# Optimization experiments

Measured on AMD Instinct MI355X. Metric: run time of the kernel, lower is better.

The kernel has to match this reference:

```python
import jax, jax.numpy as jnp
import numpy as np

N_LEVELS = 8
FEAT = 4
BASE = 512.0
MAX_RES = 32768.0
PLS_LOG2 = np.log2(MAX_RES / BASE) / (N_LEVELS - 1)  # per_level_scale exponent
PRIMES = (1, 2654435761, 805459861)  # tcnn hash primes
NUM_BASIS = 4
TIME_RES = 8


def grid_encode(x, table):
    """tcnn HashGrid encoding. x: [N, d] in [0,1]; table: [L, T, F]. Returns [N, L*F]."""
    L, T, F = table.shape
    N, d = x.shape
    feats = []
    for l in range(L):
        scale = np.exp2(l * PLS_LOG2) * BASE - 1.0  # tcnn grid_scale
        pos = x * jnp.float32(scale) + 0.5
        p0 = jnp.floor(pos)
        frac = pos - p0  # [N, d]
        p0u = p0.astype(jnp.uint32)
        acc = jnp.zeros((N, F), dtype=table.dtype)
        for corner in range(2 ** d):
            h = jnp.zeros((N,), dtype=jnp.uint32)
            w = jnp.ones((N,), dtype=pos.dtype)
            for j in range(d):
                b = (corner >> j) & 1
                c = p0u[:, j] + jnp.uint32(b)
                h = h ^ (c * jnp.uint32(PRIMES[j]))  # uint32 wraparound, as in tcnn
                w = w * (frac[:, j] if b else (1.0 - frac[:, j]))
            idx = (h & jnp.uint32(T - 1)).astype(jnp.int32)  # T is a power of 2
            acc = acc + w[:, None] * table[l][idx]
        feats.append(acc)
    return jnp.concatenate(feats, axis=-1)  # level-major layout like tcnn


def interp_basis(feat, t):
    """Lagrange multi-basis interpolation over feature chunks. feat: [N, L*F] -> [N, L*F//NUM_BASIS]."""
    N = feat.shape[0]
    f = feat.reshape(N, N_LEVELS, FEAT)
    chunks = jnp.split(f, NUM_BASIS, axis=-1)
    Tn = [i / (NUM_BASIS - 1) for i in range(NUM_BASIS)]
    out = jnp.zeros_like(chunks[0])
    for i in range(NUM_BASIS):
        coef = 1.0
        for m in range(NUM_BASIS):
            if m != i:
                coef = coef * (t - Tn[m]) / (Tn[i] - Tn[m])
        out = out + coef * chunks[i]
    return out.reshape(N, -1)


def hash_grid_t(xp, t, tables):
    """HashGridT: blend two per-time-slice 2D hash encodings, then basis-interp. tables: [TR, L, T, F]."""
    idx = t * (TIME_RES - 1)
    i1 = jnp.floor(idx).astype(jnp.int32)
    i2 = jnp.ceil(idx).astype(jnp.int32)
    w2 = idx - i1.astype(idx.dtype)
    f1 = grid_encode(xp, tables[i1])
    f2 = grid_encode(xp, tables[i2])
    feat = (1.0 - w2) * f1 + w2 * f2  # equals f1 exactly when idx is integral
    return interp_basis(feat, t)


def setup_inputs() -> dict:
    key = jax.random.key(0)
    k1, k2, k3, k4, k5, k6 = jax.random.split(key, 6)
    N = 1_000_000
    x = jax.random.uniform(k1, (N, 3), dtype=jnp.float32)
    t = jax.random.uniform(k2, (), dtype=jnp.float32)
    table_static = jax.random.normal(k3, (N_LEVELS, 2 ** 19, FEAT), dtype=jnp.float32) * 0.1
    table_xy = jax.random.normal(k4, (TIME_RES, N_LEVELS, 2 ** 15, FEAT), dtype=jnp.float32) * 0.1
    table_xz = jax.random.normal(k5, (TIME_RES, N_LEVELS, 2 ** 13, FEAT), dtype=jnp.float32) * 0.1
    table_yz = jax.random.normal(k6, (TIME_RES, N_LEVELS, 2 ** 13, FEAT), dtype=jnp.float32) * 0.1
    return {"x": x, "t": t, "table_static": table_static,
            "table_xy": table_xy, "table_xz": table_xz, "table_yz": table_yz}


def reference(x, t, table_static, table_xy, table_xz, table_yz):
    # static 3D hash grid features: [N, 32]
    feat_static = grid_encode(x, table_static)
    # dynamic tri-plane time features, concat reduction: [N, 24]
    d_xy = hash_grid_t(x[:, (0, 1)], t, table_xy)
    d_xz = hash_grid_t(x[:, (0, 2)], t, table_xz)
    d_yz = hash_grid_t(x[:, (1, 2)], t, table_yz)
    feat_dynamic = jnp.concatenate([d_xy, d_xz, d_yz], axis=-1)
    return feat_static, feat_dynamic  # decompose=True returns the pair
```

## Files before the change

### kernel.cpp

```cpp
#include <hip/hip_runtime.h>
#include <math.h>

#define NLEV 8

struct Scales { float s[NLEV]; };

__device__ __forceinline__ float4 enc2d(float pa, float pb, float s,
                                        const float* __restrict__ tbl,
                                        unsigned mask)
{
    float posa = pa * s + 0.5f;
    float posb = pb * s + 0.5f;
    float fla = floorf(posa), flb = floorf(posb);
    float fra = posa - fla, frb = posb - flb;
    unsigned ua = (unsigned)fla, ub = (unsigned)flb;
    float wa0 = 1.0f - fra, wb0 = 1.0f - frb;
    float4 acc = make_float4(0.f, 0.f, 0.f, 0.f);
#pragma unroll
    for (int c = 0; c < 4; ++c) {
        unsigned ca = ua + (c & 1);
        unsigned cb = ub + ((c >> 1) & 1);
        unsigned h = ca ^ (cb * 2654435761u);
        unsigned idx = h & mask;
        float4 v = *reinterpret_cast<const float4*>(tbl + (size_t)idx * 4u);
        float w = ((c & 1) ? fra : wa0) * (((c >> 1) & 1) ? frb : wb0);
        acc.x += w * v.x; acc.y += w * v.y; acc.z += w * v.z; acc.w += w * v.w;
    }
    return acc;
}

__global__ __launch_bounds__(256) void hg4d_kernel(
    const float* __restrict__ x,
    const float* __restrict__ tptr,
    const float* __restrict__ tstat,
    const float* __restrict__ txy,
    const float* __restrict__ txz,
    const float* __restrict__ tyz,
    float* __restrict__ outs,
    float* __restrict__ outd,
    int N, Scales sc)
{
    int n = blockIdx.x * blockDim.x + threadIdx.x;
    if (n >= N) return;
    float x0 = x[3 * (size_t)n + 0];
    float x1 = x[3 * (size_t)n + 1];
    float x2 = x[3 * (size_t)n + 2];
    float t = tptr[0];

#pragma unroll
    for (int l = 0; l < NLEV; ++l) {
        float s = sc.s[l];
        float p0 = x0 * s + 0.5f, p1 = x1 * s + 0.5f, p2 = x2 * s + 0.5f;
        float q0 = floorf(p0), q1 = floorf(p1), q2 = floorf(p2);
        float f0 = p0 - q0, f1 = p1 - q1, f2 = p2 - q2;
        unsigned u0 = (unsigned)q0, u1 = (unsigned)q1, u2 = (unsigned)q2;
        float g0 = 1.f - f0, g1 = 1.f - f1, g2 = 1.f - f2;
        const float* tb = tstat + (size_t)l * (1u << 19) * 4u;
        float4 acc = make_float4(0.f, 0.f, 0.f, 0.f);
#pragma unroll
        for (int c = 0; c < 8; ++c) {
            unsigned c0 = u0 + (c & 1);
            unsigned c1 = u1 + ((c >> 1) & 1);
            unsigned c2 = u2 + ((c >> 2) & 1);
            unsigned h = c0 ^ (c1 * 2654435761u) ^ (c2 * 805459861u);
            unsigned idx = h & ((1u << 19) - 1u);
            float4 v = *reinterpret_cast<const float4*>(tb + (size_t)idx * 4u);
            float w = ((c & 1) ? f0 : g0) * (((c >> 1) & 1) ? f1 : g1)
                    * (((c >> 2) & 1) ? f2 : g2);
            acc.x += w * v.x; acc.y += w * v.y; acc.z += w * v.z; acc.w += w * v.w;
        }
        *reinterpret_cast<float4*>(outs + (size_t)n * 32u + l * 4u) = acc;
    }

    float idxf = t * 7.0f;
    float fl = floorf(idxf);
    int i1 = (int)fl;
    int i2 = (int)ceilf(idxf);
    float w2 = idxf - fl;
    float w1 = 1.0f - w2;

    float Tn[4] = {0.f, 1.f / 3.f, 2.f / 3.f, 1.f};
    float coef[4];
#pragma unroll
    for (int i = 0; i < 4; ++i) {
        float c = 1.0f;
#pragma unroll
        for (int m = 0; m < 4; ++m)
            if (m != i) c = c * (t - Tn[m]) / (Tn[i] - Tn[m]);
        coef[i] = c;
    }

    float od[24];

    auto plane = [&](float pa, float pb, const float* __restrict__ tbl,
                     unsigned Tsz, int ob) {
        const float* b1 = tbl + (size_t)i1 * NLEV * Tsz * 4u;
        const float* b2 = tbl + (size_t)i2 * NLEV * Tsz * 4u;
#pragma unroll
        for (int l = 0; l < NLEV; ++l) {
            float s = sc.s[l];
            const float* t1 = b1 + (size_t)l * Tsz * 4u;
            const float* t2 = b2 + (size_t)l * Tsz * 4u;
            float4 a = enc2d(pa, pb, s, t1, Tsz - 1u);
            float4 b = enc2d(pa, pb, s, t2, Tsz - 1u);
            float bx = w1 * a.x + w2 * b.x;
            float by = w1 * a.y + w2 * b.y;
            float bz = w1 * a.z + w2 * b.z;
            float bw = w1 * a.w + w2 * b.w;
            float o = coef[0] * bx;
            o = o + coef[1] * by;
            o = o + coef[2] * bz;
            o = o + coef[3] * bw;
            od[ob + l] = o;
        }
    };
    plane(x0, x1, txy, 1u << 15, 0);
    plane(x0, x2, txz, 1u << 13, 8);
    plane(x1, x2, tyz, 1u << 13, 16);

    float* op = outd + (size_t)n * 24u;
#pragma unroll
    for (int k = 0; k < 6; ++k) {
        float4 v = make_float4(od[4 * k], od[4 * k + 1], od[4 * k + 2], od[4 * k + 3]);
        *reinterpret_cast<float4*>(op + 4 * k) = v;
    }
}

extern "C" void kernel_launch(void* const* d_in, const int* in_sizes, int n_in,
                              void* d_out, int out_size, void* d_ws, size_t ws_size,
                              hipStream_t stream) {
    const float* x     = (const float*)d_in[0];
    const float* tptr  = (const float*)d_in[1];
    const float* tstat = (const float*)d_in[2];
    const float* txy   = (const float*)d_in[3];
    const float* txz   = (const float*)d_in[4];
    const float* tyz   = (const float*)d_in[5];
    int N = in_sizes[0] / 3;
    float* outs = (float*)d_out;
    float* outd = outs + (size_t)N * 32u;

    Scales sc;
    const double pls = 6.0 / 7.0;
    for (int l = 0; l < NLEV; ++l)
        sc.s[l] = (float)(exp2((double)l * pls) * 512.0 - 1.0);

    dim3 block(256);
    dim3 grid((N + 255) / 256);
    hipLaunchKernelGGL(hg4d_kernel, grid, block, 0, stream,
                       x, tptr, tstat, txy, txz, tyz, outs, outd, N, sc);
}
```

Measured before the change: 1.499 ms.

## Split per-point encoding into 32 threads, one per level/plane task

Each point is now handled by 32 threads instead of one. Lanes 0-7 compute one static 3D hash level each, and lanes 8-31 compute one (plane, level) dynamic feature each. This exposes far more independent gathers at once and cuts per-thread register pressure, which should help hide the latency of the random hash-table loads. The cost is that every lane reloads x and t, and lanes 0-7 and 8-31 follow different paths within a wavefront. Hash products are also hoisted out of the corner loops.

```diff
diff --git a/kernel.cpp b/kernel.cpp
--- a/kernel.cpp
+++ b/kernel.cpp
@@ -5,31 +5,7 @@
 
 struct Scales { float s[NLEV]; };
 
-__device__ __forceinline__ float4 enc2d(float pa, float pb, float s,
-                                        const float* __restrict__ tbl,
-                                        unsigned mask)
-{
-    float posa = pa * s + 0.5f;
-    float posb = pb * s + 0.5f;
-    float fla = floorf(posa), flb = floorf(posb);
-    float fra = posa - fla, frb = posb - flb;
-    unsigned ua = (unsigned)fla, ub = (unsigned)flb;
-    float wa0 = 1.0f - fra, wb0 = 1.0f - frb;
-    float4 acc = make_float4(0.f, 0.f, 0.f, 0.f);
-#pragma unroll
-    for (int c = 0; c < 4; ++c) {
-        unsigned ca = ua + (c & 1);
-        unsigned cb = ub + ((c >> 1) & 1);
-        unsigned h = ca ^ (cb * 2654435761u);
-        unsigned idx = h & mask;
-        float4 v = *reinterpret_cast<const float4*>(tbl + (size_t)idx * 4u);
-        float w = ((c & 1) ? fra : wa0) * (((c >> 1) & 1) ? frb : wb0);
-        acc.x += w * v.x; acc.y += w * v.y; acc.z += w * v.z; acc.w += w * v.w;
-    }
-    return acc;
-}
-
-__global__ __launch_bounds__(256) void hg4d_kernel(
+__global__ __launch_bounds__(256) void hg4d_split_kernel(
     const float* __restrict__ x,
     const float* __restrict__ tptr,
     const float* __restrict__ tstat,
@@ -40,15 +16,17 @@
     float* __restrict__ outd,
     int N, Scales sc)
 {
-    int n = blockIdx.x * blockDim.x + threadIdx.x;
-    if (n >= N) return;
+    unsigned tid = blockIdx.x * blockDim.x + threadIdx.x;
+    unsigned n = tid >> 5;
+    unsigned task = tid & 31u;
+    if (n >= (unsigned)N) return;
+
     float x0 = x[3 * (size_t)n + 0];
     float x1 = x[3 * (size_t)n + 1];
     float x2 = x[3 * (size_t)n + 2];
-    float t = tptr[0];
 
-#pragma unroll
-    for (int l = 0; l < NLEV; ++l) {
+    if (task < 8u) {
+        const unsigned l = task;
         float s = sc.s[l];
         float p0 = x0 * s + 0.5f, p1 = x1 * s + 0.5f, p2 = x2 * s + 0.5f;
         float q0 = floorf(p0), q1 = floorf(p1), q2 = floorf(p2);
@@ -56,73 +34,65 @@
         unsigned u0 = (unsigned)q0, u1 = (unsigned)q1, u2 = (unsigned)q2;
         float g0 = 1.f - f0, g1 = 1.f - f1, g2 = 1.f - f2;
         const float* tb = tstat + (size_t)l * (1u << 19) * 4u;
-        float4 acc = make_float4(0.f, 0.f, 0.f, 0.f);
+        unsigned h1a = u1 * 2654435761u;
+        unsigned h1b = (u1 + 1u) * 2654435761u;
+        unsigned h2a = u2 * 805459861u;
+        unsigned h2b = (u2 + 1u) * 805459861u;
+        float ax = 0.f, ay = 0.f, az = 0.f, aw = 0.f;
 #pragma unroll
         for (int c = 0; c < 8; ++c) {
-            unsigned c0 = u0 + (c & 1);
-            unsigned c1 = u1 + ((c >> 1) & 1);
-            unsigned c2 = u2 + ((c >> 2) & 1);
-            unsigned h = c0 ^ (c1 * 2654435761u) ^ (c2 * 805459861u);
-            unsigned idx = h & ((1u << 19) - 1u);
+            unsigned hh = (u0 + (c & 1)) ^ ((c & 2) ? h1b : h1a) ^ ((c & 4) ? h2b : h2a);
+            unsigned idx = hh & ((1u << 19) - 1u);
             float4 v = *reinterpret_cast<const float4*>(tb + (size_t)idx * 4u);
-            float w = ((c & 1) ? f0 : g0) * (((c >> 1) & 1) ? f1 : g1)
-                    * (((c >> 2) & 1) ? f2 : g2);
-            acc.x += w * v.x; acc.y += w * v.y; acc.z += w * v.z; acc.w += w * v.w;
+            float w = ((c & 1) ? f0 : g0) * ((c & 2) ? f1 : g1) * ((c & 4) ? f2 : g2);
+            ax += w * v.x; ay += w * v.y; az += w * v.z; aw += w * v.w;
         }
-        *reinterpret_cast<float4*>(outs + (size_t)n * 32u + l * 4u) = acc;
-    }
+        *reinterpret_cast<float4*>(outs + (size_t)n * 32u + l * 4u) =
+            make_float4(ax, ay, az, aw);
+    } else {
+        unsigned dt = task - 8u;
+        unsigned pl = dt >> 3, l = dt & 7u;
+        float t = tptr[0];
+        float idxf = t * 7.0f;
+        float flq = floorf(idxf);
+        int i1 = (int)flq;
+        int i2 = (int)ceilf(idxf);
+        float w2 = idxf - flq, w1 = 1.0f - w2;
 
-    float idxf = t * 7.0f;
-    float fl = floorf(idxf);
-    int i1 = (int)fl;
-    int i2 = (int)ceilf(idxf);
-    float w2 = idxf - fl;
-    float w1 = 1.0f - w2;
+        const float T1 = 1.f / 3.f, T2 = 2.f / 3.f;
+        float a0 = t, a1 = t - T1, a2 = t - T2, a3 = t - 1.f;
+        float c0 = (a1 / (0.f - T1)) * (a2 / (0.f - T2)) * (a3 / (0.f - 1.f));
+        float c1 = (a0 / (T1 - 0.f)) * (a2 / (T1 - T2)) * (a3 / (T1 - 1.f));
+        float c2 = (a0 / (T2 - 0.f)) * (a1 / (T2 - T1)) * (a3 / (T2 - 1.f));
+        float c3 = (a0 / (1.f - 0.f)) * (a1 / (1.f - T1)) * (a2 / (1.f - T2));
 
-    float Tn[4] = {0.f, 1.f / 3.f, 2.f / 3.f, 1.f};
-    float coef[4];
+        const float* tbl; unsigned Tsz; float pa, pb;
+        if (pl == 0u)      { tbl = txy; Tsz = 1u << 15; pa = x0; pb = x1; }
+        else if (pl == 1u) { tbl = txz; Tsz = 1u << 13; pa = x0; pb = x2; }
+        else               { tbl = tyz; Tsz = 1u << 13; pa = x1; pb = x2; }
+        const float* t1 = tbl + ((size_t)i1 * NLEV + l) * (size_t)Tsz * 4u;
+        const float* t2 = tbl + ((size_t)i2 * NLEV + l) * (size_t)Tsz * 4u;
+
+        float s = sc.s[l];
+        float posa = pa * s + 0.5f, posb = pb * s + 0.5f;
+        float fa = floorf(posa), fb = floorf(posb);
+        float fra = posa - fa, frb = posb - fb;
+        unsigned ua = (unsigned)fa, ub = (unsigned)fb;
+        unsigned mask = Tsz - 1u;
+        unsigned hb0 = ub * 2654435761u, hb1 = (ub + 1u) * 2654435761u;
+        float A0 = 0.f, A1 = 0.f, A2 = 0.f, A3 = 0.f;
 #pragma unroll
-    for (int i = 0; i < 4; ++i) {
-        float c = 1.0f;
-#pragma unroll
-        for (int m = 0; m < 4; ++m)
-            if (m != i) c = c * (t - Tn[m]) / (Tn[i] - Tn[m]);
-        coef[i] = c;
-    }
-
-    float od[24];
-
-    auto plane = [&](float pa, float pb, const float* __restrict__ tbl,
-                     unsigned Tsz, int ob) {
-        const float* b1 = tbl + (size_t)i1 * NLEV * Tsz * 4u;
-        const float* b2 = tbl + (size_t)i2 * NLEV * Tsz * 4u;
-#pragma unroll
-        for (int l = 0; l < NLEV; ++l) {
-            float s = sc.s[l];
-            const float* t1 = b1 + (size_t)l * Tsz * 4u;
-            const float* t2 = b2 + (size_t)l * Tsz * 4u;
-            float4 a = enc2d(pa, pb, s, t1, Tsz - 1u);
-            float4 b = enc2d(pa, pb, s, t2, Tsz - 1u);
-            float bx = w1 * a.x + w2 * b.x;
-            float by = w1 * a.y + w2 * b.y;
-            float bz = w1 * a.z + w2 * b.z;
-            float bw = w1 * a.w + w2 * b.w;
-            float o = coef[0] * bx;
-            o = o + coef[1] * by;
-            o = o + coef[2] * bz;
-            o = o + coef[3] * bw;
-            od[ob + l] = o;
+        for (int c = 0; c < 4; ++c) {
+            unsigned idx = ((ua + (c & 1)) ^ ((c & 2) ? hb1 : hb0)) & mask;
+            float4 v1 = *reinterpret_cast<const float4*>(t1 + (size_t)idx * 4u);
+            float4 v2 = *reinterpret_cast<const float4*>(t2 + (size_t)idx * 4u);
+            float w = ((c & 1) ? fra : 1.f - fra) * ((c & 2) ? frb : 1.f - frb);
+            A0 += w * (w1 * v1.x + w2 * v2.x);
+            A1 += w * (w1 * v1.y + w2 * v2.y);
+            A2 += w * (w1 * v1.z + w2 * v2.z);
+            A3 += w * (w1 * v1.w + w2 * v2.w);
         }
-    };
-    plane(x0, x1, txy, 1u << 15, 0);
-    plane(x0, x2, txz, 1u << 13, 8);
-    plane(x1, x2, tyz, 1u << 13, 16);
-
-    float* op = outd + (size_t)n * 24u;
-#pragma unroll
-    for (int k = 0; k < 6; ++k) {
-        float4 v = make_float4(od[4 * k], od[4 * k + 1], od[4 * k + 2], od[4 * k + 3]);
-        *reinterpret_cast<float4*>(op + 4 * k) = v;
+        outd[(size_t)n * 24u + dt] = c0 * A0 + c1 * A1 + c2 * A2 + c3 * A3;
     }
 }
 
@@ -144,8 +114,9 @@
     for (int l = 0; l < NLEV; ++l)
         sc.s[l] = (float)(exp2((double)l * pls) * 512.0 - 1.0);
 
+    long long total = (long long)N * 32ll;
     dim3 block(256);
-    dim3 grid((N + 255) / 256);
-    hipLaunchKernelGGL(hg4d_kernel, grid, block, 0, stream,
+    dim3 grid((unsigned)((total + 255) / 256));
+    hipLaunchKernelGGL(hg4d_split_kernel, grid, block, 0, stream,
                        x, tptr, tstat, txy, txz, tyz, outs, outd, N, sc);
 }
```

Result: slower. 2.060 ms (+37.4%).
